# Optimization experiments

Hardware: AMD Instinct MI355X
Metric: run time of the kernel (lower is better)

## Reference

```python
import jax, jax.numpy as jnp
import numpy as np

V, E, H, L, B, T = 50000, 512, 512, 32, 64, 512


def _lstm_dir(xg, w_hh, reverse):
    # xg: [B,T,4H] precomputed input-to-gate projections (+ biases)
    b, t, g4 = xg.shape
    h_dim = g4 // 4
    def step(carry, xt):
        h, c = carry
        g = xt + h @ w_hh.T  # [B,4H], PyTorch gate order i,f,g,o
        i, f, gg, o = jnp.split(g, 4, axis=-1)
        c = jax.nn.sigmoid(f) * c + jax.nn.sigmoid(i) * jnp.tanh(gg)
        h = jax.nn.sigmoid(o) * jnp.tanh(c)
        return (h, c), h
    init = (jnp.zeros((b, h_dim), xg.dtype), jnp.zeros((b, h_dim), xg.dtype))
    _, hs = jax.lax.scan(step, init, jnp.swapaxes(xg, 0, 1), reverse=reverse)
    return jnp.swapaxes(hs, 0, 1)  # [B,T,H]


def _bilstm(x, w_ih0, w_ih1, w_hh, b_ih, b_hh):
    w_ihs = (w_ih0, w_ih1)
    for l in range(2):
        outs = []
        for d in range(2):  # 0=forward, 1=backward
            xg = jnp.einsum('bti,gi->btg', x, w_ihs[l][d]) + b_ih[l, d] + b_hh[l, d]
            outs.append(_lstm_dir(xg, w_hh[l, d], reverse=(d == 1)))
        x = jnp.concatenate(outs, axis=-1)  # [B,T,2H]
    return x


def _crf_nll(emissions, tags, start, end, trans):
    # pytorch-crf: returns sum log-likelihood; module returns its negation.
    emit = jnp.take_along_axis(emissions, tags[..., None], axis=-1)[..., 0]  # [B,T]
    num = (start[tags[:, 0]] + emit.sum(1)
           + trans[tags[:, :-1], tags[:, 1:]].sum(1) + end[tags[:, -1]])
    alpha0 = start + emissions[:, 0]  # [B,L]
    def step(alpha, e_t):
        s = alpha[:, :, None] + trans[None] + e_t[:, None, :]  # [B,L,L]
        return jax.nn.logsumexp(s, axis=1), None
    alpha, _ = jax.lax.scan(step, alpha0, jnp.swapaxes(emissions[:, 1:], 0, 1))
    denom = jax.nn.logsumexp(alpha + end, axis=-1)  # [B]
    return -(num - denom).sum()


def setup_inputs() -> dict:
    key = jax.random.key(0)
    ks = jax.random.split(key, 13)
    s = 0.05
    emb = jax.random.normal(ks[0], (V, E), jnp.float32) * s
    emb = emb.at[0].set(0.0)  # padding_idx=0
    return {
        'datas': jax.random.randint(ks[1], (B, T), 0, V, jnp.int32),
        'labels': jax.random.randint(ks[2], (B, T), 0, L, jnp.int32),
        'emb': emb,
        'w_ih0': jax.random.normal(ks[3], (2, 4 * H, E), jnp.float32) * s,
        'w_ih1': jax.random.normal(ks[4], (2, 4 * H, 2 * H), jnp.float32) * s,
        'w_hh': jax.random.normal(ks[5], (2, 2, 4 * H, H), jnp.float32) * s,
        'b_ih': jax.random.normal(ks[6], (2, 2, 4 * H), jnp.float32) * s,
        'b_hh': jax.random.normal(ks[7], (2, 2, 4 * H), jnp.float32) * s,
        'w_out': jax.random.normal(ks[8], (2 * H, L), jnp.float32) * s,
        'b_out': jax.random.normal(ks[9], (L,), jnp.float32) * s,
        'crf_start': jax.random.normal(ks[10], (L,), jnp.float32) * s,
        'crf_end': jax.random.normal(ks[11], (L,), jnp.float32) * s,
        'crf_trans': jax.random.normal(ks[12], (L, L), jnp.float32) * s,
    }


def reference(datas, labels, emb, w_ih0, w_ih1, w_hh, b_ih, b_hh, w_out, b_out,
              crf_start, crf_end, crf_trans):
    x = emb[datas]  # [B,T,E]
    h = _bilstm(x, w_ih0, w_ih1, w_hh, b_ih, b_hh)  # [B,T,2H]; dropout=0 (eval)
    emissions = h @ w_out + b_out  # [B,T,L]
    return _crf_nll(emissions, labels, crf_start, crf_end, crf_trans)
```

## Files before the change

kernel.cpp:

```cpp
#include <hip/hip_runtime.h>

typedef unsigned short ushort_t;
typedef unsigned long long u64_t;
typedef __attribute__((ext_vector_type(8))) short short8;
typedef __attribute__((ext_vector_type(4))) float floatx4;


__device__ __forceinline__ float bf2f(ushort_t u) {
  unsigned x = ((unsigned)u) << 16;
  return __builtin_bit_cast(float, x);
}
__device__ __forceinline__ ushort_t f2bf(float f) {
  unsigned x = __builtin_bit_cast(unsigned, f);
  x += 0x7FFFu + ((x >> 16) & 1u);
  return (ushort_t)(x >> 16);
}
__device__ __forceinline__ float sigf(float x) { return 1.0f / (1.0f + __expf(-x)); }
__device__ __forceinline__ float tanhf_(float x) { return 1.0f - 2.0f / (__expf(2.0f * x) + 1.0f); }

static const size_t OFF_A    = 0;
static const size_t OFF_OUT0 = 67108864;
static const size_t OFF_XG   = 134217728;
static const size_t OFF_WIH0 = 167772160;
static const size_t OFF_WIH1 = 171966464;
static const size_t OFF_BIAS = 180355072;
static const size_t OFF_WOUT = 180387840;
static const size_t OFF_HC   = 180453376;
static const size_t OFF_CST  = 181501952;
static const size_t OFF_BAR  = 182026240;
static const size_t OFF_NUM  = 182059008;
static const size_t OFF_PERB = 182059264;
static const size_t OFF_END  = 182059520;

__global__ void prep_kernel(const float* __restrict__ w_ih0, const float* __restrict__ w_ih1,
                            const float* __restrict__ b_ih, const float* __restrict__ b_hh,
                            const float* __restrict__ w_out,
                            ushort_t* __restrict__ wih0_bf, ushort_t* __restrict__ wih1_bf,
                            float* __restrict__ bias, ushort_t* __restrict__ wout_bf) {
  int idx = blockIdx.x * 256 + threadIdx.x;
  int stride = gridDim.x * 256;
  for (int i = idx; i < 2097152; i += stride) wih0_bf[i] = f2bf(w_ih0[i]);
  for (int i = idx; i < 4194304; i += stride) wih1_bf[i] = f2bf(w_ih1[i]);
  for (int i = idx; i < 8192; i += stride) bias[i] = b_ih[i] + b_hh[i];
  for (int i = idx; i < 32768; i += stride) {
    int j = i & 7, Ls = (i >> 3) & 63, kb = (i >> 9) & 31, nt = i >> 14;
    int n = nt * 16 + (Ls & 15);
    int k = kb * 32 + ((Ls >> 4) & 3) * 8 + j;
    wout_bf[i] = f2bf(w_out[k * 32 + n]);
  }
}

__global__ void embed_kernel(const int* __restrict__ datas, const float* __restrict__ emb,
                             ushort_t* __restrict__ x_bf) {
  int idx = blockIdx.x * 256 + threadIdx.x;
  int row = idx >> 6, sub = idx & 63;
  int tok = datas[row];
  const float4* ep = (const float4*)(emb + (size_t)tok * 512 + sub * 8);
  float4 f0 = ep[0], f1 = ep[1];
  short8 v;
  v[0] = (short)f2bf(f0.x); v[1] = (short)f2bf(f0.y);
  v[2] = (short)f2bf(f0.z); v[3] = (short)f2bf(f0.w);
  v[4] = (short)f2bf(f1.x); v[5] = (short)f2bf(f1.y);
  v[6] = (short)f2bf(f1.z); v[7] = (short)f2bf(f1.w);
  *(short8*)(x_bf + (size_t)row * 512 + sub * 8) = v;
}

__global__ __launch_bounds__(256) void gemm_chunk(const ushort_t* __restrict__ A, int K,
                                                  const ushort_t* __restrict__ W,
                                                  const float* __restrict__ biasL,
                                                  ushort_t* __restrict__ xg0c,
                                                  ushort_t* __restrict__ xg1c,
                                                  int t00, int t01) {
  __shared__ alignas(16) ushort_t alds[512 * 8];
  __shared__ alignas(16) ushort_t blds[512 * 8];
  int gid = blockIdx.x;
  int dir = gid >> 9, r = gid & 511;
  int mt = r & 31, ntt = r >> 5;
  int t0 = dir ? t01 : t00;
  const ushort_t* Bm = W + (size_t)dir * 2048 * K;
  const float* bptr = biasL + dir * 2048;
  ushort_t* xg = dir ? xg1c : xg0c;
  int bm0 = mt * 128, bn0 = ntt * 128;
  int tid = threadIdx.x, L = tid & 63, w = tid >> 6;
  int wm = w & 1, wn = w >> 1;
  floatx4 acc[4][4] = {};
  for (int k0 = 0; k0 < K; k0 += 32) {
    __syncthreads();
    #pragma unroll
    for (int rep = 0; rep < 2; rep++) {
      int slot = rep * 256 + tid;
      int t8 = slot >> 6, Ls = slot & 63;
      int col = k0 + (Ls >> 4) * 8;
      int mp = bm0 + t8 * 16 + (Ls & 15);
      int Arow = (mp >> 6) * 512 + t0 + (mp & 63);
      *(short8*)&alds[slot * 8] = *(const short8*)&A[(size_t)Arow * K + col];
      int rowb = bn0 + t8 * 16 + (Ls & 15);
      *(short8*)&blds[slot * 8] = *(const short8*)&Bm[(size_t)rowb * K + col];
    }
    __syncthreads();
    short8 af[4];
    #pragma unroll
    for (int a = 0; a < 4; a++) af[a] = *(const short8*)&alds[((wm * 4 + a) * 64 + L) * 8];
    #pragma unroll
    for (int bq = 0; bq < 4; bq++) {
      short8 bfr = *(const short8*)&blds[((wn * 4 + bq) * 64 + L) * 8];
      #pragma unroll
      for (int a = 0; a < 4; a++)
        acc[a][bq] = __builtin_amdgcn_mfma_f32_16x16x32_bf16(af[a], bfr, acc[a][bq], 0, 0, 0);
    }
  }
  int lm = L >> 4, ln = L & 15;
  #pragma unroll
  for (int bq = 0; bq < 4; bq++) {
    int n = bn0 + (wn * 4 + bq) * 16 + ln;
    float bv = bptr[n];
    #pragma unroll
    for (int a = 0; a < 4; a++) {
      #pragma unroll
      for (int rr = 0; rr < 4; rr++) {
        int m = bm0 + (wm * 4 + a) * 16 + lm * 4 + rr;
        int b = m >> 6, ts = m & 63;
        xg[((size_t)(ts * 64 + b)) * 2048 + n] = f2bf(acc[a][bq][rr] + bv);
      }
    }
  }
}

__global__ __launch_bounds__(256) void lstm_chunk(const ushort_t* __restrict__ xg0c,
                                                  const ushort_t* __restrict__ xg1c,
                                                  const float* __restrict__ whh_f,
                                                  ushort_t* __restrict__ hcL,
                                                  float* __restrict__ cstL,
                                                  ushort_t* __restrict__ outL,
                                                  int* __restrict__ barF, int c) {
  __shared__ alignas(16) ushort_t wlds[32768];
  int bid = blockIdx.x, d = bid >> 5, g = bid & 31, j0 = g * 16;
  int tid = threadIdx.x, L = tid & 63, w = tid >> 6;
  const float* wptr = whh_f + (size_t)d * 2048 * 512;
  #pragma unroll
  for (int it = 0; it < 16; it++) {
    int slot = it * 256 + tid;
    int q = slot >> 10, kb = (slot >> 6) & 15, Ls = slot & 63;
    int gcol = q * 512 + j0 + (Ls & 15);
    int k = kb * 32 + (Ls >> 4) * 8;
    const float* src = wptr + (size_t)gcol * 512 + k;
    float4 f0 = *(const float4*)src;
    float4 f1 = *(const float4*)(src + 4);
    short8 v;
    v[0] = (short)f2bf(f0.x); v[1] = (short)f2bf(f0.y);
    v[2] = (short)f2bf(f0.z); v[3] = (short)f2bf(f0.w);
    v[4] = (short)f2bf(f1.x); v[5] = (short)f2bf(f1.y);
    v[6] = (short)f2bf(f1.z); v[7] = (short)f2bf(f1.w);
    *(short8*)&wlds[slot * 8] = v;
  }
  __syncthreads();
  const ushort_t* xgd = d ? xg1c : xg0c;
  ushort_t* hcd = hcL + (size_t)d * 2 * 32768;
  int* flg = barF + d * 2048;
  int* myflag = flg + (g * 4 + w) * 16;
  const int* pollp = flg + ((L & 31) * 4 + w) * 16;
  bool pact = (L < 32);
  int q8 = L >> 4, jj = L & 15;
  int mbase = w * 16 + q8 * 4;
  int wslot = ((w * 16 + (g >> 1)) * 64 + q8 * 4 + 16 * ((g & 1) * 2 + (jj >> 3))) * 8 + (jj & 7);
  int rbase = (w * 16 * 64 + L) * 8;
  float cv[4];
  #pragma unroll
  for (int rr = 0; rr < 4; rr++) cv[rr] = cstL[(size_t)d * 32768 + (mbase + rr) * 512 + j0 + jj];

  auto ldxg = [&](int sl2, ushort_t dst[4][4]) {
    int ts2 = d ? (63 - sl2) : sl2;
    #pragma unroll
    for (int rr = 0; rr < 4; rr++) {
      const ushort_t* xrow = xgd + ((size_t)(ts2 * 64 + mbase + rr)) * 2048 + j0 + jj;
      #pragma unroll
      for (int q = 0; q < 4; q++) dst[q][rr] = xrow[q * 512];
    }
  };

  ushort_t xgu[4][4];
  ldxg(0, xgu);

  for (int sl = 0; sl < 64; sl++) {
    int s = c * 64 + sl;
    int t = d ? (511 - s) : s;
    const u64_t* h64 = (const u64_t*)(hcd + (size_t)(s & 1) * 32768);
    unsigned* h32w = (unsigned*)(hcd + (size_t)((s + 1) & 1) * 32768);
    int b64 = rbase >> 2;
    u64_t hv[32];
    #pragma unroll
    for (int kb = 0; kb < 16; kb++) {
      hv[2 * kb]     = __hip_atomic_load(h64 + b64 + kb * 128,     __ATOMIC_RELAXED, __HIP_MEMORY_SCOPE_AGENT);
      hv[2 * kb + 1] = __hip_atomic_load(h64 + b64 + kb * 128 + 1, __ATOMIC_RELAXED, __HIP_MEMORY_SCOPE_AGENT);
    }
    floatx4 acc[4] = {};
    #pragma unroll
    for (int kb = 0; kb < 16; kb++) {
      union { u64_t u[2]; short8 v; } pk;
      pk.u[0] = hv[2 * kb];
      pk.u[1] = hv[2 * kb + 1];
      short8 a = pk.v;
      #pragma unroll
      for (int q = 0; q < 4; q++) {
        short8 bfr = *(const short8*)&wlds[((q * 16 + kb) * 64 + L) * 8];
        acc[q] = __builtin_amdgcn_mfma_f32_16x16x32_bf16(a, bfr, acc[q], 0, 0, 0);
      }
    }
    ushort_t hbv[4];
    #pragma unroll
    for (int rr = 0; rr < 4; rr++) {
      float ii = acc[0][rr] + bf2f(xgu[0][rr]);
      float ff = acc[1][rr] + bf2f(xgu[1][rr]);
      float gg = acc[2][rr] + bf2f(xgu[2][rr]);
      float oo = acc[3][rr] + bf2f(xgu[3][rr]);
      float cc = sigf(ff) * cv[rr] + sigf(ii) * tanhf_(gg);
      cv[rr] = cc;
      hbv[rr] = f2bf(sigf(oo) * tanhf_(cc));
    }
    bool evn = (jj & 1) == 0;
    unsigned pk4[4];
    #pragma unroll
    for (int rr = 0; rr < 4; rr++) {
      unsigned mine = (unsigned)hbv[rr];
      unsigned nb = (unsigned)__shfl_xor((int)mine, 1, 64);
      pk4[rr] = mine | (nb << 16);
      if (evn)
        __hip_atomic_store(h32w + ((wslot + rr * 8) >> 1), pk4[rr],
                           __ATOMIC_RELAXED, __HIP_MEMORY_SCOPE_AGENT);
    }
    if (sl != 63) {
      asm volatile("s_waitcnt vmcnt(0)" ::: "memory");
      if (L == 0)
        __hip_atomic_store(myflag, s + 1, __ATOMIC_RELAXED, __HIP_MEMORY_SCOPE_AGENT);
      if (evn) {
        #pragma unroll
        for (int rr = 0; rr < 4; rr++) {
          int m = mbase + rr;
          *(unsigned*)&outL[((size_t)m * 512 + t) * 1024 + (d << 9) + j0 + jj] = pk4[rr];
        }
      }
      ldxg(sl + 1, xgu);
      int target = s + 1, guard = 0;
      while (guard < (1 << 17)) {
        int f = pact ? __hip_atomic_load(pollp, __ATOMIC_RELAXED, __HIP_MEMORY_SCOPE_AGENT)
                     : target;
        if (__ballot(f >= target) == ~0ULL) break;
        guard++;
      }
    } else {
      if (evn) {
        #pragma unroll
        for (int rr = 0; rr < 4; rr++) {
          int m = mbase + rr;
          *(unsigned*)&outL[((size_t)m * 512 + t) * 1024 + (d << 9) + j0 + jj] = pk4[rr];
        }
      }
    }
  }
  #pragma unroll
  for (int rr = 0; rr < 4; rr++) cstL[(size_t)d * 32768 + (mbase + rr) * 512 + j0 + jj] = cv[rr];
}

__global__ __launch_bounds__(256) void emis_kernel(const ushort_t* __restrict__ out1,
                                                   const ushort_t* __restrict__ wout_bf,
                                                   const float* __restrict__ b_out,
                                                   float* __restrict__ emis) {
  int tid = threadIdx.x, L = tid & 63, w = tid >> 6;
  int bm0 = blockIdx.x * 128;
  int q8 = L >> 4, ln = L & 15;
  floatx4 acc[2][2] = {};
  #pragma unroll 4
  for (int kb = 0; kb < 32; kb++) {
    short8 a0 = *(const short8*)&out1[(size_t)(bm0 + (w * 2 + 0) * 16 + ln) * 1024 + kb * 32 + q8 * 8];
    short8 a1 = *(const short8*)&out1[(size_t)(bm0 + (w * 2 + 1) * 16 + ln) * 1024 + kb * 32 + q8 * 8];
    #pragma unroll
    for (int nt = 0; nt < 2; nt++) {
      short8 bfr = *(const short8*)&wout_bf[((size_t)(nt * 32 + kb) * 64 + L) * 8];
      acc[0][nt] = __builtin_amdgcn_mfma_f32_16x16x32_bf16(a0, bfr, acc[0][nt], 0, 0, 0);
      acc[1][nt] = __builtin_amdgcn_mfma_f32_16x16x32_bf16(a1, bfr, acc[1][nt], 0, 0, 0);
    }
  }
  #pragma unroll
  for (int mt = 0; mt < 2; mt++) {
    #pragma unroll
    for (int nt = 0; nt < 2; nt++) {
      int n = nt * 16 + ln;
      float bv = b_out[n];
      #pragma unroll
      for (int rr = 0; rr < 4; rr++) {
        int m = bm0 + (w * 2 + mt) * 16 + q8 * 4 + rr;
        emis[(size_t)m * 32 + n] = acc[mt][nt][rr] + bv;
      }
    }
  }
}

__global__ void num_kernel(const int* __restrict__ labels, const float* __restrict__ emis,
                           const float* __restrict__ trans, const float* __restrict__ cstart,
                           const float* __restrict__ cend, float* __restrict__ num) {
  int b = blockIdx.x, tid = threadIdx.x;
  float s = 0.f;
  for (int t = tid; t < 512; t += 64) {
    int tag = labels[b * 512 + t];
    s += emis[(size_t)(b * 512 + t) * 32 + tag];
    if (t < 511) s += trans[tag * 32 + labels[b * 512 + t + 1]];
  }
  #pragma unroll
  for (int off = 32; off > 0; off >>= 1) s += __shfl_xor(s, off, 64);
  if (tid == 0) num[b] = s + cstart[labels[b * 512]] + cend[labels[b * 512 + 511]];
}

__global__ __launch_bounds__(64) void fwd_kernel(const float* __restrict__ emis,
                                                 const float* __restrict__ trans,
                                                 const float* __restrict__ cstart,
                                                 const float* __restrict__ cend,
                                                 const float* __restrict__ num,
                                                 float* __restrict__ perb) {
  int b = blockIdx.x, tid = threadIdx.x, j = tid & 31;
  float etr[32];
  #pragma unroll
  for (int i = 0; i < 32; i++) etr[i] = __expf(trans[i * 32 + j]);
  float alpha = cstart[j] + emis[(size_t)(b * 512) * 32 + j];
  float e_cur = emis[(size_t)(b * 512 + 1) * 32 + j];
  for (int t = 1; t < 512; t++) {
    float e_nx = (t < 511) ? emis[(size_t)(b * 512 + t + 1) * 32 + j] : 0.f;
    float mA = alpha;
    mA = fmaxf(mA, __shfl_xor(mA, 1, 32));
    mA = fmaxf(mA, __shfl_xor(mA, 2, 32));
    mA = fmaxf(mA, __shfl_xor(mA, 4, 32));
    mA = fmaxf(mA, __shfl_xor(mA, 8, 32));
    mA = fmaxf(mA, __shfl_xor(mA, 16, 32));
    float p = __expf(alpha - mA);
    float s0 = 0.f, s1 = 0.f, s2 = 0.f, s3 = 0.f;
    #pragma unroll
    for (int i = 0; i < 32; i += 4) {
      s0 = fmaf(__shfl(p, i, 32),     etr[i],     s0);
      s1 = fmaf(__shfl(p, i + 1, 32), etr[i + 1], s1);
      s2 = fmaf(__shfl(p, i + 2, 32), etr[i + 2], s2);
      s3 = fmaf(__shfl(p, i + 3, 32), etr[i + 3], s3);
    }
    alpha = __logf((s0 + s1) + (s2 + s3)) + mA + e_cur;
    e_cur = e_nx;
  }
  float z = alpha + cend[j];
  float m2 = z;
  #pragma unroll
  for (int off = 16; off > 0; off >>= 1) m2 = fmaxf(m2, __shfl_xor(m2, off, 32));
  float s2r = __expf(z - m2);
  #pragma unroll
  for (int off = 16; off > 0; off >>= 1) s2r += __shfl_xor(s2r, off, 32);
  if (tid == 0) perb[b] = num[b] - (__logf(s2r) + m2);
}

__global__ void final_kernel(const float* __restrict__ perb, float* __restrict__ out) {
  int tid = threadIdx.x;
  float s = perb[tid];
  #pragma unroll
  for (int off = 32; off > 0; off >>= 1) s += __shfl_xor(s, off, 64);
  if (tid == 0) out[0] = -s;
}

extern "C" void kernel_launch(void* const* d_in, const int* in_sizes, int n_in,
                              void* d_out, int out_size, void* d_ws, size_t ws_size,
                              hipStream_t stream) {
  (void)in_sizes; (void)n_in; (void)out_size; (void)ws_size;
  const int* datas = (const int*)d_in[0];
  const int* labels = (const int*)d_in[1];
  const float* emb = (const float*)d_in[2];
  const float* w_ih0 = (const float*)d_in[3];
  const float* w_ih1 = (const float*)d_in[4];
  const float* w_hh = (const float*)d_in[5];
  const float* b_ih = (const float*)d_in[6];
  const float* b_hh = (const float*)d_in[7];
  const float* w_out = (const float*)d_in[8];
  const float* b_out = (const float*)d_in[9];
  const float* cstart = (const float*)d_in[10];
  const float* cend = (const float*)d_in[11];
  const float* ctrans = (const float*)d_in[12];

  char* ws = (char*)d_ws;
  ushort_t* x_bf = (ushort_t*)(ws + OFF_A);
  ushort_t* out1 = (ushort_t*)(ws + OFF_A);
  ushort_t* out0 = (ushort_t*)(ws + OFF_OUT0);
  ushort_t* xg0c = (ushort_t*)(ws + OFF_XG);
  ushort_t* xg1c = (ushort_t*)(ws + OFF_XG + 16777216);
  float* emis = (float*)(ws + OFF_XG);
  ushort_t* wih0_bf = (ushort_t*)(ws + OFF_WIH0);
  ushort_t* wih1_bf = (ushort_t*)(ws + OFF_WIH1);
  float* bias = (float*)(ws + OFF_BIAS);
  ushort_t* wout_bf = (ushort_t*)(ws + OFF_WOUT);
  ushort_t* hc0 = (ushort_t*)(ws + OFF_HC);
  ushort_t* hc1 = hc0 + 131072;
  float* cst0 = (float*)(ws + OFF_CST);
  float* cst1 = cst0 + 65536;
  int* bar = (int*)(ws + OFF_BAR);
  float* numb = (float*)(ws + OFF_NUM);
  float* perb = (float*)(ws + OFF_PERB);

  hipMemsetAsync(ws + OFF_HC, 0, OFF_END - OFF_HC, stream);

  prep_kernel<<<2048, 256, 0, stream>>>(w_ih0, w_ih1, b_ih, b_hh, w_out,
                                        wih0_bf, wih1_bf, bias, wout_bf);
  embed_kernel<<<8192, 256, 0, stream>>>(datas, emb, x_bf);

  for (int c = 0; c < 8; c++) {
    gemm_chunk<<<1024, 256, 0, stream>>>(x_bf, 512, wih0_bf, bias, xg0c, xg1c,
                                         c * 64, (7 - c) * 64);
    lstm_chunk<<<64, 256, 0, stream>>>(xg0c, xg1c, w_hh, hc0, cst0, out0, bar, c);
  }
  for (int c = 0; c < 8; c++) {
    gemm_chunk<<<1024, 256, 0, stream>>>(out0, 1024, wih1_bf, bias + 4096, xg0c, xg1c,
                                         c * 64, (7 - c) * 64);
    lstm_chunk<<<64, 256, 0, stream>>>(xg0c, xg1c, w_hh + 2097152, hc1, cst1, out1,
                                       bar + 4096, c);
  }

  emis_kernel<<<256, 256, 0, stream>>>(out1, wout_bf, b_out, emis);
  num_kernel<<<64, 64, 0, stream>>>(labels, emis, ctrans, cstart, cend, numb);
  fwd_kernel<<<64, 64, 0, stream>>>(emis, ctrans, cstart, cend, numb, perb);
  final_kernel<<<1, 64, 0, stream>>>(perb, (float*)d_out);
}
```

Before: 5.519 ms.

## Overlap next-chunk input GEMM with LSTM recurrence in a fused launch

Splits the GEMM and LSTM kernels into device-side bodies and adds a fused kernel. In it, the first 64 blocks run the recurrent LSTM chunk while the remaining blocks compute the input-gate projections for the next time chunk. The xg buffers are double-buffered so the projection GEMM no longer serialises with the latency-bound recurrence and can use idle CUs. For layer 1 the double buffer goes past OFF_END and is used only when the workspace is large enough; otherwise it falls back to sequential launches. The fused kernel reserves 64KB of LDS per block, which may lower GEMM occupancy. It also depends on the spin-waiting LSTM blocks staying co-resident.

```diff
diff --git a/kernel.cpp b/kernel.cpp
--- a/kernel.cpp
+++ b/kernel.cpp
@@ -65,23 +65,21 @@
   *(short8*)(x_bf + (size_t)row * 512 + sub * 8) = v;
 }
 
-__global__ __launch_bounds__(256) void gemm_chunk(const ushort_t* __restrict__ A, int K,
-                                                  const ushort_t* __restrict__ W,
-                                                  const float* __restrict__ biasL,
-                                                  ushort_t* __restrict__ xg0c,
-                                                  ushort_t* __restrict__ xg1c,
-                                                  int t00, int t01) {
-  __shared__ alignas(16) ushort_t alds[512 * 8];
-  __shared__ alignas(16) ushort_t blds[512 * 8];
-  int gid = blockIdx.x;
+__device__ __forceinline__ void gemm_body(ushort_t* alds, ushort_t* blds, int gid, int tid,
+                                          const ushort_t* __restrict__ A, int K,
+                                          const ushort_t* __restrict__ W,
+                                          const float* __restrict__ biasL,
+                                          ushort_t* __restrict__ xg0,
+                                          ushort_t* __restrict__ xg1,
+                                          int t00, int t01) {
   int dir = gid >> 9, r = gid & 511;
   int mt = r & 31, ntt = r >> 5;
   int t0 = dir ? t01 : t00;
   const ushort_t* Bm = W + (size_t)dir * 2048 * K;
   const float* bptr = biasL + dir * 2048;
-  ushort_t* xg = dir ? xg1c : xg0c;
+  ushort_t* xg = dir ? xg1 : xg0;
   int bm0 = mt * 128, bn0 = ntt * 128;
-  int tid = threadIdx.x, L = tid & 63, w = tid >> 6;
+  int L = tid & 63, w = tid >> 6;
   int wm = w & 1, wn = w >> 1;
   floatx4 acc[4][4] = {};
   for (int k0 = 0; k0 < K; k0 += 32) {
@@ -126,16 +124,27 @@
   }
 }
 
-__global__ __launch_bounds__(256) void lstm_chunk(const ushort_t* __restrict__ xg0c,
-                                                  const ushort_t* __restrict__ xg1c,
-                                                  const float* __restrict__ whh_f,
-                                                  ushort_t* __restrict__ hcL,
-                                                  float* __restrict__ cstL,
-                                                  ushort_t* __restrict__ outL,
-                                                  int* __restrict__ barF, int c) {
-  __shared__ alignas(16) ushort_t wlds[32768];
-  int bid = blockIdx.x, d = bid >> 5, g = bid & 31, j0 = g * 16;
-  int tid = threadIdx.x, L = tid & 63, w = tid >> 6;
+__global__ __launch_bounds__(256) void gemm_chunk(const ushort_t* __restrict__ A, int K,
+                                                  const ushort_t* __restrict__ W,
+                                                  const float* __restrict__ biasL,
+                                                  ushort_t* __restrict__ xg0c,
+                                                  ushort_t* __restrict__ xg1c,
+                                                  int t00, int t01) {
+  __shared__ alignas(16) ushort_t alds[512 * 8];
+  __shared__ alignas(16) ushort_t blds[512 * 8];
+  gemm_body(alds, blds, blockIdx.x, threadIdx.x, A, K, W, biasL, xg0c, xg1c, t00, t01);
+}
+
+__device__ __forceinline__ void lstm_body(ushort_t* wlds, int bid, int tid,
+                                          const ushort_t* __restrict__ xg0c,
+                                          const ushort_t* __restrict__ xg1c,
+                                          const float* __restrict__ whh_f,
+                                          ushort_t* __restrict__ hcL,
+                                          float* __restrict__ cstL,
+                                          ushort_t* __restrict__ outL,
+                                          int* __restrict__ barF, int c) {
+  int d = bid >> 5, g = bid & 31, j0 = g * 16;
+  int L = tid & 63, w = tid >> 6;
   const float* wptr = whh_f + (size_t)d * 2048 * 512;
   #pragma unroll
   for (int it = 0; it < 16; it++) {
@@ -261,6 +270,35 @@
   for (int rr = 0; rr < 4; rr++) cstL[(size_t)d * 32768 + (mbase + rr) * 512 + j0 + jj] = cv[rr];
 }
 
+__global__ __launch_bounds__(256) void lstm_chunk(const ushort_t* __restrict__ xg0c,
+                                                  const ushort_t* __restrict__ xg1c,
+                                                  const float* __restrict__ whh_f,
+                                                  ushort_t* __restrict__ hcL,
+                                                  float* __restrict__ cstL,
+                                                  ushort_t* __restrict__ outL,
+                                                  int* __restrict__ barF, int c) {
+  __shared__ alignas(16) ushort_t wlds[32768];
+  lstm_body(wlds, blockIdx.x, threadIdx.x, xg0c, xg1c, whh_f, hcL, cstL, outL, barF, c);
+}
+
+__global__ __launch_bounds__(256) void fused_chunk(
+    const ushort_t* __restrict__ l_xg0, const ushort_t* __restrict__ l_xg1,
+    const float* __restrict__ whh_f, ushort_t* __restrict__ hcL,
+    float* __restrict__ cstL, ushort_t* __restrict__ outL,
+    int* __restrict__ barF, int c,
+    const ushort_t* __restrict__ g_A, int g_K,
+    const ushort_t* __restrict__ g_W, const float* __restrict__ g_bias,
+    ushort_t* __restrict__ g_xg0, ushort_t* __restrict__ g_xg1,
+    int g_t00, int g_t01) {
+  __shared__ alignas(16) ushort_t lds[32768];
+  if (blockIdx.x < 64) {
+    lstm_body(lds, blockIdx.x, threadIdx.x, l_xg0, l_xg1, whh_f, hcL, cstL, outL, barF, c);
+  } else {
+    gemm_body(lds, lds + 4096, blockIdx.x - 64, threadIdx.x,
+              g_A, g_K, g_W, g_bias, g_xg0, g_xg1, g_t00, g_t01);
+  }
+}
+
 __global__ __launch_bounds__(256) void emis_kernel(const ushort_t* __restrict__ out1,
                                                    const ushort_t* __restrict__ wout_bf,
                                                    const float* __restrict__ b_out,
@@ -363,7 +401,7 @@
 extern "C" void kernel_launch(void* const* d_in, const int* in_sizes, int n_in,
                               void* d_out, int out_size, void* d_ws, size_t ws_size,
                               hipStream_t stream) {
-  (void)in_sizes; (void)n_in; (void)out_size; (void)ws_size;
+  (void)in_sizes; (void)n_in; (void)out_size;
   const int* datas = (const int*)d_in[0];
   const int* labels = (const int*)d_in[1];
   const float* emb = (const float*)d_in[2];
@@ -382,8 +420,13 @@
   ushort_t* x_bf = (ushort_t*)(ws + OFF_A);
   ushort_t* out1 = (ushort_t*)(ws + OFF_A);
   ushort_t* out0 = (ushort_t*)(ws + OFF_OUT0);
-  ushort_t* xg0c = (ushort_t*)(ws + OFF_XG);
-  ushort_t* xg1c = (ushort_t*)(ws + OFF_XG + 16777216);
+  ushort_t* xA0 = (ushort_t*)(ws + OFF_XG);
+  ushort_t* xA1 = (ushort_t*)(ws + OFF_XG + 16777216);
+  ushort_t* xB0a = (ushort_t*)(ws + OFF_A + 33554432);
+  ushort_t* xB0b = (ushort_t*)(ws + OFF_A + 50331648);
+  ushort_t* xB1a = (ushort_t*)(ws + OFF_END);
+  ushort_t* xB1b = (ushort_t*)(ws + OFF_END + 16777216);
+  bool big = ws_size >= OFF_END + 33554432ull;
   float* emis = (float*)(ws + OFF_XG);
   ushort_t* wih0_bf = (ushort_t*)(ws + OFF_WIH0);
   ushort_t* wih1_bf = (ushort_t*)(ws + OFF_WIH1);
@@ -403,16 +446,44 @@
                                         wih0_bf, wih1_bf, bias, wout_bf);
   embed_kernel<<<8192, 256, 0, stream>>>(datas, emb, x_bf);
 
+  gemm_chunk<<<1024, 256, 0, stream>>>(x_bf, 512, wih0_bf, bias, xA0, xA1, 0, 448);
   for (int c = 0; c < 8; c++) {
-    gemm_chunk<<<1024, 256, 0, stream>>>(x_bf, 512, wih0_bf, bias, xg0c, xg1c,
-                                         c * 64, (7 - c) * 64);
-    lstm_chunk<<<64, 256, 0, stream>>>(xg0c, xg1c, w_hh, hc0, cst0, out0, bar, c);
-  }
+    ushort_t* r0 = (c & 1) ? xB0a : xA0;
+    ushort_t* r1 = (c & 1) ? xB0b : xA1;
+    if (c < 7) {
+      ushort_t* w0 = ((c + 1) & 1) ? xB0a : xA0;
+      ushort_t* w1 = ((c + 1) & 1) ? xB0b : xA1;
+      fused_chunk<<<1088, 256, 0, stream>>>(r0, r1, w_hh, hc0, cst0, out0, bar, c,
+                                            x_bf, 512, wih0_bf, bias, w0, w1,
+                                            (c + 1) * 64, (6 - c) * 64);
+    } else {
+      lstm_chunk<<<64, 256, 0, stream>>>(r0, r1, w_hh, hc0, cst0, out0, bar, c);
+    }
+  }
+
+  gemm_chunk<<<1024, 256, 0, stream>>>(out0, 1024, wih1_bf, bias + 4096, xA0, xA1, 0, 448);
   for (int c = 0; c < 8; c++) {
-    gemm_chunk<<<1024, 256, 0, stream>>>(out0, 1024, wih1_bf, bias + 4096, xg0c, xg1c,
-                                         c * 64, (7 - c) * 64);
-    lstm_chunk<<<64, 256, 0, stream>>>(xg0c, xg1c, w_hh + 2097152, hc1, cst1, out1,
-                                       bar + 4096, c);
+    if (big) {
+      ushort_t* r0 = (c & 1) ? xB1a : xA0;
+      ushort_t* r1 = (c & 1) ? xB1b : xA1;
+      if (c < 7) {
+        ushort_t* w0 = ((c + 1) & 1) ? xB1a : xA0;
+        ushort_t* w1 = ((c + 1) & 1) ? xB1b : xA1;
+        fused_chunk<<<1088, 256, 0, stream>>>(r0, r1, w_hh + 2097152, hc1, cst1, out1,
+                                              bar + 4096, c,
+                                              out0, 1024, wih1_bf, bias + 4096, w0, w1,
+                                              (c + 1) * 64, (6 - c) * 64);
+      } else {
+        lstm_chunk<<<64, 256, 0, stream>>>(r0, r1, w_hh + 2097152, hc1, cst1, out1,
+                                           bar + 4096, c);
+      }
+    } else {
+      lstm_chunk<<<64, 256, 0, stream>>>(xA0, xA1, w_hh + 2097152, hc1, cst1, out1,
+                                         bar + 4096, c);
+      if (c < 7)
+        gemm_chunk<<<1024, 256, 0, stream>>>(out0, 1024, wih1_bf, bias + 4096, xA0, xA1,
+                                             (c + 1) * 64, (6 - c) * 64);
+    }
   }
 
   emis_kernel<<<256, 256, 0, stream>>>(out1, wout_bf, b_out, emis);
```

After: 4.919 ms. -10.9%, faster.
